# Performance work log

Hardware: AMD Instinct MI355X
Metric: run time of the kernel (lower is better)

Reference implementation:

```python
import jax, jax.numpy as jnp
import numpy as np

B, T, D, K = 32, 1024, 256, 1024


def setup_inputs() -> dict:
    key = jax.random.key(0)
    k1, k2 = jax.random.split(key)
    z_e_x = jax.random.normal(k1, (B, T, D), dtype=jnp.float32)
    # codebook initialized uniform(-1/K, 1/K) as in VQEmbedding.__init__
    codebook = jax.random.uniform(k2, (K, D), minval=-1.0 / K, maxval=1.0 / K, dtype=jnp.float32)
    return {"z_e_x": z_e_x, "codebook": codebook}


def _vq_indices(x_flat, codebook):
    c_sqr = jnp.sum(codebook * codebook, axis=1)            # [K]
    x_sqr = jnp.sum(x_flat * x_flat, axis=1, keepdims=True)  # [N,1]
    dist = c_sqr[None, :] + x_sqr - 2.0 * (x_flat @ codebook.T)  # [N,K]
    return jnp.argmin(dist, axis=1)                          # [N]


def reference(z_e_x, codebook):
    # VQEmbedding.straight_through with slice=1 (forward values)
    shp = z_e_x.shape
    x_flat = z_e_x.reshape(-1, codebook.shape[1])            # [N,D]
    idx = _vq_indices(x_flat, codebook)                      # [N] int
    codes = codebook[idx].reshape(shp)                       # gather lookup
    # z_q_x and z_q_x_bar are numerically identical (differ only in grad path);
    # also return the indices (what VQEmbedding.forward returns)
    return codes, codes, idx.reshape(shp[:-1])
```

## Files before the change

### kernel.cpp

```cpp
#include <hip/hip_runtime.h>


#define NROWS  32768
#define DDIM   256
#define KCODES 1024
#define MARGIN 1.5e-3f
#define CAP    1024
#define RPB    64
#define XPITCH 260

typedef __attribute__((ext_vector_type(8))) short short8;
typedef __attribute__((ext_vector_type(4))) float f32x4;

__device__ __forceinline__ unsigned short f2bf(float f) {
    unsigned u = __float_as_uint(f);
    return (unsigned short)((u + 0x7FFFu + ((u >> 16) & 1u)) >> 16);
}

__device__ __forceinline__ float exact_dot(const float* __restrict__ xrow,
                                           const float* __restrict__ crow) {
    const float4* xp = (const float4*)xrow;
    const float4* cp = (const float4*)crow;
    float A = 0.f, B = 0.f;
    #pragma unroll 8
    for (int d4 = 0; d4 < 32; ++d4) {
        float4 xv = xp[d4], cv = cp[d4];
        A = __fmaf_rn(xv.x, cv.x, A);
        A = __fmaf_rn(xv.y, cv.y, A);
        A = __fmaf_rn(xv.z, cv.z, A);
        A = __fmaf_rn(xv.w, cv.w, A);
    }
    #pragma unroll 8
    for (int d4 = 32; d4 < 64; ++d4) {
        float4 xv = xp[d4], cv = cp[d4];
        B = __fmaf_rn(xv.x, cv.x, B);
        B = __fmaf_rn(xv.y, cv.y, B);
        B = __fmaf_rn(xv.z, cv.z, B);
        B = __fmaf_rn(xv.w, cv.w, B);
    }
    return __fadd_rn(A, B);
}

__global__ __launch_bounds__(256) void vq_csqr(const float* __restrict__ cb,
                                               float* __restrict__ csqr) {
    int gid  = blockIdx.x * 256 + threadIdx.x;
    int w    = gid >> 6;
    int lane = threadIdx.x & 63;
    if (w >= KCODES) return;
    float4 v = reinterpret_cast<const float4*>(cb)[w * (DDIM / 4) + lane];
    float s = v.x * v.x + v.y * v.y + v.z * v.z + v.w * v.w;
    #pragma unroll
    for (int off = 32; off > 0; off >>= 1) s += __shfl_down(s, off, 64);
    if (lane == 0) csqr[w] = s;
}

__global__ __launch_bounds__(256) void vq_xsqr(const float* __restrict__ x,
                                               float* __restrict__ xsqr) {
    int w = threadIdx.x >> 6, lane = threadIdx.x & 63;
    int row = blockIdx.x * 4 + w;
    float4 v = reinterpret_cast<const float4*>(x + (size_t)row * DDIM)[lane];
    float s = v.x * v.x + v.y * v.y + v.z * v.z + v.w * v.w;
    #pragma unroll
    for (int off = 32; off > 0; off >>= 1) s += __shfl_down(s, off, 64);
    if (lane == 0) xsqr[row] = s;
}

__global__ __launch_bounds__(256) void vq_cbfrag(const float* __restrict__ cb,
                                                 short* __restrict__ cbh) {
    int id   = blockIdx.x * 256 + threadIdx.x;
    int lane = id & 63;
    int ks   = (id >> 6) & 7;
    int nt   = id >> 9;
    int code = nt * 16 + (lane & 15);
    int d0   = ks * 32 + (lane >> 4) * 8;
    const float4* p = (const float4*)(cb + (size_t)code * DDIM + d0);
    float4 a = p[0], b = p[1];
    short8 v;
    v[0] = (short)f2bf(a.x); v[1] = (short)f2bf(a.y);
    v[2] = (short)f2bf(a.z); v[3] = (short)f2bf(a.w);
    v[4] = (short)f2bf(b.x); v[5] = (short)f2bf(b.y);
    v[6] = (short)f2bf(b.z); v[7] = (short)f2bf(b.w);
    *(short8*)(cbh + (size_t)id * 8) = v;
}

__device__ __forceinline__ f32x4 dot_tile(const short8 (&afr)[8],
                                          const short8* __restrict__ cbh8,
                                          int nt, int lane) {
    const short8* bp = cbh8 + (size_t)nt * 8 * 64 + lane;
    short8 bv[8];
    #pragma unroll
    for (int ks = 0; ks < 8; ++ks) bv[ks] = bp[(size_t)ks * 64];
    f32x4 af = (f32x4){0.f, 0.f, 0.f, 0.f};
    #pragma unroll
    for (int ks = 0; ks < 8; ++ks)
        af = __builtin_amdgcn_mfma_f32_16x16x32_bf16(afr[ks], bv[ks], af, 0, 0, 0);
    return af;
}

__global__ __launch_bounds__(512, 4) void vq_main(const float* __restrict__ x,
                                                  const float* __restrict__ cb,
                                                  const short* __restrict__ cbh,
                                                  const float* __restrict__ csqr,
                                                  const float* __restrict__ xsqr,
                                                  float* __restrict__ out) {
    __shared__ float              xl[RPB * XPITCH];
    __shared__ float              csl[KCODES];
    __shared__ unsigned           kred[8][16];
    __shared__ float              thrsh[RPB];
    __shared__ unsigned long long keys[RPB];
    __shared__ unsigned           list[CAP];
    __shared__ int                fidx[RPB];
    __shared__ int                cnt, ovf;

    const int t    = threadIdx.x;
    const int lane = t & 63;
    const int w    = t >> 6;
    const int tile = w >> 1;
    const int q    = w & 1;
    const int r0   = blockIdx.x * RPB;
    const int lr   = lane & 15;
    const int lg   = lane >> 4;

    if (t < 256) ((float4*)csl)[t] = ((const float4*)csqr)[t];
    if (t < RPB) keys[t] = ~0ULL;
    if (t == 0) { cnt = 0; ovf = 0; }

    {
        const float4* xg = (const float4*)(x + (size_t)r0 * DDIM);
        #pragma unroll
        for (int kk = 0; kk < 8; ++kk) {
            int i   = kk * 512 + t;
            int row = i >> 6, c4 = i & 63;
            float4 v = xg[i];
            *(float4*)&xl[row * XPITCH + c4 * 4] = v;
        }
    }
    __syncthreads();

    short8 afr[8];
    {
        const float* xr = &xl[(tile * 16 + lr) * XPITCH];
        #pragma unroll
        for (int ks = 0; ks < 8; ++ks) {
            float4 a = *(const float4*)&xr[ks * 32 + lg * 8];
            float4 b = *(const float4*)&xr[ks * 32 + lg * 8 + 4];
            short8 v;
            v[0] = (short)f2bf(a.x); v[1] = (short)f2bf(a.y);
            v[2] = (short)f2bf(a.z); v[3] = (short)f2bf(a.w);
            v[4] = (short)f2bf(b.x); v[5] = (short)f2bf(b.y);
            v[6] = (short)f2bf(b.z); v[7] = (short)f2bf(b.w);
            afr[ks] = v;
        }
    }

    const short8* cbh8 = (const short8*)cbh;

    unsigned run[4] = {~0u, ~0u, ~0u, ~0u};
    for (int nn = 0; nn < 32; ++nn) {
        int nt = q * 32 + nn;
        f32x4 af = dot_tile(afr, cbh8, nt, lane);
        int   code = nt * 16 + lr;
        float cs1  = __fadd_rn(csl[code], 1.0f);
        #pragma unroll
        for (int j = 0; j < 4; ++j) {
            float s = __fmaf_rn(-2.f, af[j], cs1);
            unsigned kp = (__float_as_uint(s) & 0xFFFFFC00u) | (unsigned)code;
            run[j] = run[j] < kp ? run[j] : kp;
        }
    }
    #pragma unroll
    for (int j = 0; j < 4; ++j) {
        unsigned v = run[j];
        #pragma unroll
        for (int m = 1; m < 16; m <<= 1) {
            unsigned o = __shfl_xor(v, m, 64);
            v = o < v ? o : v;
        }
        run[j] = v;
    }
    if (lr == 0) {
        #pragma unroll
        for (int j = 0; j < 4; ++j) kred[w][lg * 4 + j] = run[j];
    }
    __syncthreads();
    if (t < RPB) {
        int tl = t >> 4, rr = t & 15;
        unsigned a = kred[tl * 2][rr], b = kred[tl * 2 + 1][rr];
        unsigned m = a < b ? a : b;
        thrsh[t] = __uint_as_float(m & 0xFFFFFC00u) + MARGIN;
    }
    __syncthreads();

    for (int nn = 0; nn < 32; ++nn) {
        int nt = q * 32 + nn;
        f32x4 af = dot_tile(afr, cbh8, nt, lane);
        int   code = nt * 16 + lr;
        float cs1  = __fadd_rn(csl[code], 1.0f);
        #pragma unroll
        for (int j = 0; j < 4; ++j) {
            float s   = __fmaf_rn(-2.f, af[j], cs1);
            int   row = tile * 16 + lg * 4 + j;
            if (s <= thrsh[row]) {
                int pos = atomicAdd(&cnt, 1);
                if (pos < CAP) list[pos] = ((unsigned)row << 10) | (unsigned)code;
                else ovf = 1;
            }
        }
    }
    __syncthreads();

    if (ovf || cnt > CAP) {
        for (int it = t; it < RPB * KCODES; it += 512) {
            int row = it >> 10, code = it & (KCODES - 1);
            float dot = exact_dot(&xl[row * XPITCH], cb + (size_t)code * DDIM);
            float s   = __fmaf_rn(-2.f, dot, __fadd_rn(csl[code], xsqr[r0 + row]));
            atomicMin(&keys[row], ((unsigned long long)__float_as_uint(s) << 32) | (unsigned)code);
        }
    } else {
        for (int i = t; i < cnt; i += 512) {
            unsigned e = list[i];
            int row = (int)(e >> 10), code = (int)(e & 0x3FFu);
            float dot = exact_dot(&xl[row * XPITCH], cb + (size_t)code * DDIM);
            float s   = __fmaf_rn(-2.f, dot, __fadd_rn(csl[code], xsqr[r0 + row]));
            atomicMin(&keys[row], ((unsigned long long)__float_as_uint(s) << 32) | (unsigned)code);
        }
    }
    __syncthreads();

    if (t < RPB) {
        int code = (int)(unsigned)(keys[t] & 0xffffffffu);
        fidx[t] = code;
        out[(size_t)2 * NROWS * DDIM + (r0 + t)] = (float)code;
    }
    __syncthreads();

    const float4* cb4  = (const float4*)cb;
    float4*       out0 = (float4*)out;
    float4*       out1 = out0 + (size_t)NROWS * (DDIM / 4);
    #pragma unroll
    for (int i = 0; i < 8; ++i) {
        int it  = i * 512 + t;
        int row = it >> 6, col = it & 63;
        float4 v = cb4[(size_t)fidx[row] * (DDIM / 4) + col];
        size_t o = (size_t)(r0 + row) * (DDIM / 4) + col;
        out0[o] = v;
        out1[o] = v;
    }
}

extern "C" void kernel_launch(void* const* d_in, const int* in_sizes, int n_in,
                              void* d_out, int out_size, void* d_ws, size_t ws_size,
                              hipStream_t stream) {
    const float* x   = (const float*)d_in[0];
    const float* cb  = (const float*)d_in[1];
    float*       out = (float*)d_out;

    float* ws_csqr = (float*)d_ws;
    float* ws_xsqr = ws_csqr + KCODES;
    short* ws_cbh  = (short*)(ws_xsqr + NROWS);

    vq_cbfrag<<<128,        256, 0, stream>>>(cb, ws_cbh);
    vq_csqr  <<<256,        256, 0, stream>>>(cb, ws_csqr);
    vq_xsqr  <<<NROWS / 4,  256, 0, stream>>>(x, ws_xsqr);
    vq_main  <<<NROWS / RPB, 512, 0, stream>>>(x, cb, ws_cbh, ws_csqr, ws_xsqr, out);
}
```

Measured before the change: 99.94 us.

## Stage codebook fragments through double-buffered LDS with 4 waves covering all codes

The main kernel now runs 256 threads per block. Each wave owns 16 rows and scans all 1024 codes, where before two waves split the codes per row tile. Codebook bf16 fragments are staged in chunks into a double-buffered shared-memory buffer, with register prefetch two chunks ahead, so all four waves reuse one global load. The x tile is no longer copied to LDS; A fragments and exact rescoring read x directly from global. This aims to cut redundant global/L2 codebook traffic and drop the cross-wave threshold reduction, at the cost of a barrier per chunk and fewer waves per block.

After: 94.05 us. 1.06x faster.

```diff
diff --git a/kernel.cpp b/kernel.cpp
--- a/kernel.cpp
+++ b/kernel.cpp
@@ -7,7 +7,7 @@
 #define MARGIN 1.5e-3f
 #define CAP    1024
 #define RPB    64
-#define XPITCH 260
+#define NCHUNK 16
 
 typedef __attribute__((ext_vector_type(8))) short short8;
 typedef __attribute__((ext_vector_type(4))) float f32x4;
@@ -83,30 +83,14 @@
     *(short8*)(cbh + (size_t)id * 8) = v;
 }
 
-__device__ __forceinline__ f32x4 dot_tile(const short8 (&afr)[8],
-                                          const short8* __restrict__ cbh8,
-                                          int nt, int lane) {
-    const short8* bp = cbh8 + (size_t)nt * 8 * 64 + lane;
-    short8 bv[8];
-    #pragma unroll
-    for (int ks = 0; ks < 8; ++ks) bv[ks] = bp[(size_t)ks * 64];
-    f32x4 af = (f32x4){0.f, 0.f, 0.f, 0.f};
-    #pragma unroll
-    for (int ks = 0; ks < 8; ++ks)
-        af = __builtin_amdgcn_mfma_f32_16x16x32_bf16(afr[ks], bv[ks], af, 0, 0, 0);
-    return af;
-}
-
-__global__ __launch_bounds__(512, 4) void vq_main(const float* __restrict__ x,
+__global__ __launch_bounds__(256, 2) void vq_main(const float* __restrict__ x,
                                                   const float* __restrict__ cb,
                                                   const short* __restrict__ cbh,
                                                   const float* __restrict__ csqr,
                                                   const float* __restrict__ xsqr,
                                                   float* __restrict__ out) {
-    __shared__ float              xl[RPB * XPITCH];
+    __shared__ short              bstage[2][4 * 8 * 64 * 8];
     __shared__ float              csl[KCODES];
-    __shared__ unsigned           kred[8][16];
-    __shared__ float              thrsh[RPB];
     __shared__ unsigned long long keys[RPB];
     __shared__ unsigned           list[CAP];
     __shared__ int                fidx[RPB];
@@ -115,31 +99,17 @@
     const int t    = threadIdx.x;
     const int lane = t & 63;
     const int w    = t >> 6;
-    const int tile = w >> 1;
-    const int q    = w & 1;
     const int r0   = blockIdx.x * RPB;
     const int lr   = lane & 15;
     const int lg   = lane >> 4;
 
-    if (t < 256) ((float4*)csl)[t] = ((const float4*)csqr)[t];
+    ((float4*)csl)[t] = ((const float4*)csqr)[t];
     if (t < RPB) keys[t] = ~0ULL;
     if (t == 0) { cnt = 0; ovf = 0; }
 
-    {
-        const float4* xg = (const float4*)(x + (size_t)r0 * DDIM);
-        #pragma unroll
-        for (int kk = 0; kk < 8; ++kk) {
-            int i   = kk * 512 + t;
-            int row = i >> 6, c4 = i & 63;
-            float4 v = xg[i];
-            *(float4*)&xl[row * XPITCH + c4 * 4] = v;
-        }
-    }
-    __syncthreads();
-
     short8 afr[8];
     {
-        const float* xr = &xl[(tile * 16 + lr) * XPITCH];
+        const float* xr = x + (size_t)(r0 + w * 16 + lr) * DDIM;
         #pragma unroll
         for (int ks = 0; ks < 8; ++ks) {
             float4 a = *(const float4*)&xr[ks * 32 + lg * 8];
@@ -155,72 +125,97 @@
 
     const short8* cbh8 = (const short8*)cbh;
 
-    unsigned run[4] = {~0u, ~0u, ~0u, ~0u};
-    for (int nn = 0; nn < 32; ++nn) {
-        int nt = q * 32 + nn;
-        f32x4 af = dot_tile(afr, cbh8, nt, lane);
-        int   code = nt * 16 + lr;
-        float cs1  = __fadd_rn(csl[code], 1.0f);
-        #pragma unroll
-        for (int j = 0; j < 4; ++j) {
-            float s = __fmaf_rn(-2.f, af[j], cs1);
-            unsigned kp = (__float_as_uint(s) & 0xFFFFFC00u) | (unsigned)code;
-            run[j] = run[j] < kp ? run[j] : kp;
-        }
-    }
-    #pragma unroll
-    for (int j = 0; j < 4; ++j) {
-        unsigned v = run[j];
-        #pragma unroll
-        for (int m = 1; m < 16; m <<= 1) {
-            unsigned o = __shfl_xor(v, m, 64);
-            v = o < v ? o : v;
-        }
-        run[j] = v;
-    }
-    if (lr == 0) {
-        #pragma unroll
-        for (int j = 0; j < 4; ++j) kred[w][lg * 4 + j] = run[j];
+    short8 pf[8];
+    #pragma unroll
+    for (int i = 0; i < 8; ++i) pf[i] = cbh8[(size_t)0 * 2048 + i * 256 + t];
+    {
+        short8* dst = (short8*)bstage[0];
+        #pragma unroll
+        for (int i = 0; i < 8; ++i) dst[i * 256 + t] = pf[i];
+        #pragma unroll
+        for (int i = 0; i < 8; ++i) pf[i] = cbh8[(size_t)1 * 2048 + i * 256 + t];
     }
     __syncthreads();
-    if (t < RPB) {
-        int tl = t >> 4, rr = t & 15;
-        unsigned a = kred[tl * 2][rr], b = kred[tl * 2 + 1][rr];
-        unsigned m = a < b ? a : b;
-        thrsh[t] = __uint_as_float(m & 0xFFFFFC00u) + MARGIN;
-    }
-    __syncthreads();
-
-    for (int nn = 0; nn < 32; ++nn) {
-        int nt = q * 32 + nn;
-        f32x4 af = dot_tile(afr, cbh8, nt, lane);
-        int   code = nt * 16 + lr;
-        float cs1  = __fadd_rn(csl[code], 1.0f);
-        #pragma unroll
-        for (int j = 0; j < 4; ++j) {
-            float s   = __fmaf_rn(-2.f, af[j], cs1);
-            int   row = tile * 16 + lg * 4 + j;
-            if (s <= thrsh[row]) {
-                int pos = atomicAdd(&cnt, 1);
-                if (pos < CAP) list[pos] = ((unsigned)row << 10) | (unsigned)code;
-                else ovf = 1;
+
+    unsigned runp[4];
+    #pragma unroll
+    for (int j = 0; j < 4; ++j) runp[j] = ~0u;
+    float thr[4];
+
+    for (int c = 0; c < 2 * NCHUNK; ++c) {
+        const int q = c & (NCHUNK - 1);
+        if (c + 1 < 2 * NCHUNK) {
+            short8* dst = (short8*)bstage[(c + 1) & 1];
+            #pragma unroll
+            for (int i = 0; i < 8; ++i) dst[i * 256 + t] = pf[i];
+        }
+        if (c + 2 < 2 * NCHUNK) {
+            const size_t cb2 = (size_t)((c + 2) & (NCHUNK - 1)) * 2048;
+            #pragma unroll
+            for (int i = 0; i < 8; ++i) pf[i] = cbh8[cb2 + i * 256 + t];
+        }
+        const short* bs = bstage[c & 1];
+        #pragma unroll
+        for (int m = 0; m < 4; ++m) {
+            const int nt = q * 4 + m;
+            short8 bv[8];
+            #pragma unroll
+            for (int ks = 0; ks < 8; ++ks)
+                bv[ks] = *(const short8*)&bs[((m * 8 + ks) * 64 + lane) * 8];
+            f32x4 af = (f32x4){0.f, 0.f, 0.f, 0.f};
+            #pragma unroll
+            for (int ks = 0; ks < 8; ++ks)
+                af = __builtin_amdgcn_mfma_f32_16x16x32_bf16(afr[ks], bv[ks], af, 0, 0, 0);
+
+            const int code = nt * 16 + lr;
+            float cs1 = __fadd_rn(csl[code], 1.0f);
+            if (c < NCHUNK) {
+                #pragma unroll
+                for (int j = 0; j < 4; ++j) {
+                    float s = __fmaf_rn(-2.f, af[j], cs1);
+                    unsigned kp = (__float_as_uint(s) & 0xFFFFFC00u) | (unsigned)code;
+                    runp[j] = runp[j] < kp ? runp[j] : kp;
+                }
+            } else {
+                #pragma unroll
+                for (int j = 0; j < 4; ++j) {
+                    float s = __fmaf_rn(-2.f, af[j], cs1);
+                    if (s <= thr[j]) {
+                        int row = w * 16 + lg * 4 + j;
+                        int pos = atomicAdd(&cnt, 1);
+                        if (pos < CAP) list[pos] = ((unsigned)row << 10) | (unsigned)code;
+                        else ovf = 1;
+                    }
+                }
             }
         }
-    }
-    __syncthreads();
+        if (c == NCHUNK - 1) {
+            #pragma unroll
+            for (int j = 0; j < 4; ++j) {
+                unsigned v = runp[j];
+                #pragma unroll
+                for (int mm = 1; mm < 16; mm <<= 1) {
+                    unsigned o = __shfl_xor(v, mm, 64);
+                    v = o < v ? o : v;
+                }
+                thr[j] = __uint_as_float(v & 0xFFFFFC00u) + MARGIN;
+            }
+        }
+        __syncthreads();
+    }
 
     if (ovf || cnt > CAP) {
-        for (int it = t; it < RPB * KCODES; it += 512) {
+        for (int it = t; it < RPB * KCODES; it += 256) {
             int row = it >> 10, code = it & (KCODES - 1);
-            float dot = exact_dot(&xl[row * XPITCH], cb + (size_t)code * DDIM);
+            float dot = exact_dot(x + (size_t)(r0 + row) * DDIM, cb + (size_t)code * DDIM);
             float s   = __fmaf_rn(-2.f, dot, __fadd_rn(csl[code], xsqr[r0 + row]));
             atomicMin(&keys[row], ((unsigned long long)__float_as_uint(s) << 32) | (unsigned)code);
         }
     } else {
-        for (int i = t; i < cnt; i += 512) {
+        for (int i = t; i < cnt; i += 256) {
             unsigned e = list[i];
             int row = (int)(e >> 10), code = (int)(e & 0x3FFu);
-            float dot = exact_dot(&xl[row * XPITCH], cb + (size_t)code * DDIM);
+            float dot = exact_dot(x + (size_t)(r0 + row) * DDIM, cb + (size_t)code * DDIM);
             float s   = __fmaf_rn(-2.f, dot, __fadd_rn(csl[code], xsqr[r0 + row]));
             atomicMin(&keys[row], ((unsigned long long)__float_as_uint(s) << 32) | (unsigned)code);
         }
@@ -238,8 +233,8 @@
     float4*       out0 = (float4*)out;
     float4*       out1 = out0 + (size_t)NROWS * (DDIM / 4);
     #pragma unroll
-    for (int i = 0; i < 8; ++i) {
-        int it  = i * 512 + t;
+    for (int i = 0; i < 16; ++i) {
+        int it  = i * 256 + t;
         int row = it >> 6, col = it & 63;
         float4 v = cb4[(size_t)fidx[row] * (DDIM / 4) + col];
         size_t o = (size_t)(r0 + row) * (DDIM / 4) + col;
@@ -262,5 +257,5 @@
     vq_cbfrag<<<128,        256, 0, stream>>>(cb, ws_cbh);
     vq_csqr  <<<256,        256, 0, stream>>>(cb, ws_csqr);
     vq_xsqr  <<<NROWS / 4,  256, 0, stream>>>(x, ws_xsqr);
-    vq_main  <<<NROWS / RPB, 512, 0, stream>>>(x, cb, ws_cbh, ws_csqr, ws_xsqr, out);
-}
+    vq_main  <<<NROWS / RPB, 256, 0, stream>>>(x, cb, ws_cbh, ws_csqr, ws_xsqr, out);
+}
```
